# Kernel optimization log

Measured on AMD Instinct MI355X. Metric: run time of the kernel, lower is better.

## Reference

```python
import jax, jax.numpy as jnp
import numpy as np
import math

B, H, HK, Q, K, D = 2, 64, 8, 1024, 1024, 128
HIDDEN = H * D

def setup_inputs() -> dict:
    key = jax.random.key(0)
    k1, k2, k3, k4, k5 = jax.random.split(key, 5)
    xq = jax.random.normal(k1, (B, H, Q, D), dtype=jnp.float32)
    keys = jax.random.normal(k2, (B, HK, K, D), dtype=jnp.float32)
    values = jax.random.normal(k3, (B, HK, K, D), dtype=jnp.float32)
    attn_mask = jax.random.normal(k4, (B, 1, Q, K), dtype=jnp.float32)
    wo = jax.random.normal(k5, (HIDDEN, HIDDEN), dtype=jnp.float32) * 0.02
    return {"xq": xq, "keys": keys, "values": values, "attn_mask": attn_mask, "wo": wo}

def reference(xq, keys, values, attn_mask, wo):
    b, h, q, d = xq.shape
    hk = keys.shape[1]
    g = h // hk  # GQA group size
    scale = 1.0 / math.sqrt(d)
    # expand kv heads to match query heads (group_attn_matmul semantics)
    k = jnp.repeat(keys, g, axis=1)    # [b, h, K, d]
    v = jnp.repeat(values, g, axis=1)  # [b, h, K, d]
    attn = jnp.einsum('bhqd,bhkd->bhqk', xq, k) * scale + attn_mask
    attn = jax.nn.softmax(attn, axis=-1)
    out = jnp.einsum('bhqk,bhkd->bhqd', attn, v)
    # nlp_concat_heads: [b, h, q, d] -> [b, q, h*d]
    out = out.transpose(0, 2, 1, 3).reshape(b, q, h * d)
    return out @ wo
```

## Files before the change

### kernel.cpp

```cpp
#include <hip/hip_runtime.h>
#include <hip/hip_bf16.h>
#include <stdint.h>

#define NB   2
#define NH   64
#define NHK  8
#define SQ   1024
#define SK   1024
#define DH   128
#define HID  8192
#define MROWS 2048
#define NT   128

typedef unsigned short u16;
typedef __bf16 bf16_t;
typedef bf16_t bf16x8 __attribute__((ext_vector_type(8)));
typedef float  f32x4  __attribute__((ext_vector_type(4)));
typedef u16    u16x8  __attribute__((ext_vector_type(8)));
typedef u16    u16x4  __attribute__((ext_vector_type(4)));

#define DEV __device__ __forceinline__

DEV u16 f2bf(float f) {
  uint32_t u = __builtin_bit_cast(uint32_t, f);
  u += 0x7fffu + ((u >> 16) & 1u);
  return (u16)(u >> 16);
}

DEV float bf2f(u16 u) {
  return __builtin_bit_cast(float, (uint32_t)u << 16);
}

DEV bf16x8 pack8(const float* v) {
  u16x8 r;
#pragma unroll
  for (int i = 0; i < 8; ++i) r[i] = f2bf(v[i]);
  return __builtin_bit_cast(bf16x8, r);
}

DEV f32x4 mfma16(bf16x8 a, bf16x8 b, f32x4 c) {
  return __builtin_amdgcn_mfma_f32_16x16x32_bf16(a, b, c, 0, 0, 0);
}

DEV void gload_lds16(const void* g, void* l) {
  __builtin_amdgcn_global_load_lds(
      (const __attribute__((address_space(1))) void*)g,
      (__attribute__((address_space(3))) void*)l, 16, 0, 0);
}

#define BAR()  asm volatile("s_barrier" ::: "memory")
#define VMC(n) asm volatile("s_waitcnt vmcnt(" #n ")" ::: "memory")

__global__ __launch_bounds__(256) void k_prep(
    const float* __restrict__ wo, u16* __restrict__ wt,
    const float* __restrict__ keys, char* __restrict__ kf,
    const float* __restrict__ values, char* __restrict__ vf,
    const float* __restrict__ mask, u16* __restrict__ mb) {
  __shared__ float tile[64][65];
  const int bid = blockIdx.x;
  const int tid = threadIdx.x;

  if (bid < 16384) {
    const int k0 = (bid & 127) * 64;
    const int n0 = (bid >> 7) * 64;
    const int r  = tid >> 4, cg = tid & 15;
#pragma unroll
    for (int p = 0; p < 4; ++p) {
      int row = r + p * 16;
      float4 v = *(const float4*)(wo + (size_t)(k0 + row) * 8192 + n0 + cg * 4);
      *(float4*)&tile[row][cg * 4] = v;
    }
    __syncthreads();
#pragma unroll
    for (int p = 0; p < 4; ++p) {
      int row = r + p * 16;
      u16x4 ov;
      ov[0] = f2bf(tile[cg * 4 + 0][row]);
      ov[1] = f2bf(tile[cg * 4 + 1][row]);
      ov[2] = f2bf(tile[cg * 4 + 2][row]);
      ov[3] = f2bf(tile[cg * 4 + 3][row]);
      *(u16x4*)(wt + (size_t)(n0 + row) * 8192 + k0 + cg * 4) = ov;
    }
  } else if (bid < 17408) {
    int g = (bid - 16384) * 256 + tid;
    int l    = g & 63;
    int blk  = (g >> 6) & 15;
    int t    = (g >> 10) & 15;
    int head = g >> 14;
    int ni = blk >> 2, c = blk & 3;
    int row = t * 64 + ni * 16 + (l & 15);
    int col = c * 32 + (l >> 4) * 8;
    const float* src = keys + ((size_t)head * 1024 + row) * 128 + col;
    float tb[8];
    *(float4*)tb       = *(const float4*)src;
    *(float4*)(tb + 4) = *(const float4*)(src + 4);
    u16x8 r;
#pragma unroll
    for (int i = 0; i < 8; ++i) r[i] = f2bf(tb[i]);
    *(u16x8*)(kf + (size_t)g * 16) = r;
  } else if (bid < 18432) {
    int g = (bid - 17408) * 256 + tid;
    int l    = g & 63;
    int blk  = (g >> 6) & 15;
    int t    = (g >> 10) & 15;
    int head = g >> 14;
    int ks = blk >> 3, nd = blk & 7;
    int k0 = t * 64 + ks * 32 + (l >> 4) * 8;
    int d  = nd * 16 + (l & 15);
    const float* src = values + (size_t)head * 131072 + (size_t)k0 * 128 + d;
    u16x8 r;
#pragma unroll
    for (int j = 0; j < 8; ++j) r[j] = f2bf(src[j * 128]);
    *(u16x8*)(vf + (size_t)g * 16) = r;
  } else {
    int g = (bid - 18432) * 256 + tid;
    const float* src = mask + (size_t)g * 8;
    float tb[8];
    *(float4*)tb       = *(const float4*)src;
    *(float4*)(tb + 4) = *(const float4*)(src + 4);
    u16x8 r;
#pragma unroll
    for (int i = 0; i < 8; ++i) r[i] = f2bf(tb[i]);
    *(u16x8*)(mb + (size_t)g * 8) = r;
  }
}

__global__ __launch_bounds__(256) void k_attn(
    const float* __restrict__ xq, const char* __restrict__ kf_g,
    const char* __restrict__ vf_g, const u16* __restrict__ maskb,
    u16* __restrict__ abf) {
  __shared__ char smem[16384];
  const int bid = (blockIdx.x & 7) * 128 + (blockIdx.x >> 3);
  const int tid = threadIdx.x;

  const int b = bid >> 9;
  const int h = (bid >> 3) & 63;
  const int q0 = (bid & 7) * 128;
  const int hk = h >> 3;
  const int w = tid >> 6, l = tid & 63;
  const int lr = l & 15, lg = l >> 4;
  char* pbyte = smem + w * 4096;

  bf16x8 qf[2][4];
  {
    const float* qb = xq + (((size_t)(b * NH + h) * SQ) + q0 + w * 32) * DH;
#pragma unroll
    for (int mi = 0; mi < 2; ++mi)
#pragma unroll
      for (int c = 0; c < 4; ++c) {
        const float* qp = qb + (size_t)(mi * 16 + lr) * DH + c * 32 + lg * 8;
        float t[8];
        *(float4*)t       = *(const float4*)qp;
        *(float4*)(t + 4) = *(const float4*)(qp + 4);
        qf[mi][c] = pack8(t);
      }
  }

  f32x4 o[2][8];
#pragma unroll
  for (int mi = 0; mi < 2; ++mi)
#pragma unroll
    for (int nd = 0; nd < 8; ++nd) o[mi][nd] = (f32x4){0.f, 0.f, 0.f, 0.f};
  float mrun[2] = {-1e30f, -1e30f}, lrun[2] = {0.f, 0.f};

  const char* kb_base = kf_g + (size_t)(b * NHK + hk) * 262144 + l * 16;
  const char* vb_base = vf_g + (size_t)(b * NHK + hk) * 262144 + l * 16;
  const u16* mk0 = maskb + (size_t)b * SQ * SK +
                   (size_t)(q0 + w * 32 + lr) * SK + lg * 4;
  const float SCALE = 0.08838834764831845f;
  const float L2E   = 1.4426950408889634f;
  const int rswz = (lr & 7) << 4;

  for (int t = 0; t < 16; ++t) {
    const int kb = t * 64;
    const char* kt = kb_base + t * 16384;
    u16x4 mpre[2][4];
#pragma unroll
    for (int mi = 0; mi < 2; ++mi)
#pragma unroll
      for (int ni = 0; ni < 4; ++ni)
        mpre[mi][ni] = *(const u16x4*)(mk0 + (size_t)mi * 16 * SK + kb + ni * 16);

    f32x4 st[2][4];
#pragma unroll
    for (int mi = 0; mi < 2; ++mi)
#pragma unroll
      for (int ni = 0; ni < 4; ++ni) st[mi][ni] = (f32x4){0.f, 0.f, 0.f, 0.f};
    __builtin_amdgcn_s_setprio(1);
#pragma unroll
    for (int ni = 0; ni < 4; ++ni)
#pragma unroll
      for (int c = 0; c < 4; ++c) {
        bf16x8 kf = *(const bf16x8*)(kt + (ni * 4 + c) * 1024);
        st[0][ni] = mfma16(kf, qf[0][c], st[0][ni]);
        st[1][ni] = mfma16(kf, qf[1][c], st[1][ni]);
      }
    __builtin_amdgcn_s_setprio(0);

#pragma unroll
    for (int mi = 0; mi < 2; ++mi) {
      float x[4][4];
#pragma unroll
      for (int ni = 0; ni < 4; ++ni)
#pragma unroll
        for (int r = 0; r < 4; ++r)
          x[ni][r] = st[mi][ni][r] * SCALE + bf2f(mpre[mi][ni][r]);
      float v = fmaxf(fmaxf(x[0][0], x[0][1]), fmaxf(x[0][2], x[0][3]));
#pragma unroll
      for (int ni = 1; ni < 4; ++ni)
        v = fmaxf(v, fmaxf(fmaxf(x[ni][0], x[ni][1]),
                           fmaxf(x[ni][2], x[ni][3])));
      v = fmaxf(v, __shfl_xor(v, 16));
      v = fmaxf(v, __shfl_xor(v, 32));
      if (__any(v > mrun[mi] + 8.0f)) {
        float mnew = fmaxf(mrun[mi], v);
        float fac = exp2f((mrun[mi] - mnew) * L2E);
        lrun[mi] *= fac;
        mrun[mi] = mnew;
#pragma unroll
        for (int r = 0; r < 4; ++r) {
          float fr = __shfl(fac, lg * 4 + r);
#pragma unroll
          for (int nd = 0; nd < 8; ++nd) o[mi][nd][r] *= fr;
        }
      }
      float rs = 0.f;
      char* prow = pbyte + (mi * 16 + lr) * 128;
#pragma unroll
      for (int ni = 0; ni < 4; ++ni) {
        float p0 = exp2f((x[ni][0] - mrun[mi]) * L2E);
        float p1 = exp2f((x[ni][1] - mrun[mi]) * L2E);
        float p2 = exp2f((x[ni][2] - mrun[mi]) * L2E);
        float p3 = exp2f((x[ni][3] - mrun[mi]) * L2E);
        rs += (p0 + p1) + (p2 + p3);
        uint2 pk;
        pk.x = f2bf(p0) | ((uint32_t)f2bf(p1) << 16);
        pk.y = f2bf(p2) | ((uint32_t)f2bf(p3) << 16);
        *(uint2*)(prow + ((ni * 32 + lg * 8) ^ rswz)) = pk;
      }
      rs += __shfl_xor(rs, 16);
      rs += __shfl_xor(rs, 32);
      lrun[mi] += rs;
    }

    const char* vt = vb_base + t * 16384;
    __builtin_amdgcn_s_setprio(1);
#pragma unroll
    for (int ks = 0; ks < 2; ++ks) {
      bf16x8 pf0 = *(const bf16x8*)(pbyte + lr * 128 +
                                    ((ks * 64 + lg * 16) ^ rswz));
      bf16x8 pf1 = *(const bf16x8*)(pbyte + (16 + lr) * 128 +
                                    ((ks * 64 + lg * 16) ^ rswz));
#pragma unroll
      for (int nd = 0; nd < 8; ++nd) {
        bf16x8 vf = *(const bf16x8*)(vt + (ks * 8 + nd) * 1024);
        o[0][nd] = mfma16(pf0, vf, o[0][nd]);
        o[1][nd] = mfma16(pf1, vf, o[1][nd]);
      }
    }
    __builtin_amdgcn_s_setprio(0);
  }

#pragma unroll
  for (int mi = 0; mi < 2; ++mi) {
    float inv[4];
#pragma unroll
    for (int r = 0; r < 4; ++r) inv[r] = 1.0f / __shfl(lrun[mi], lg * 4 + r);
#pragma unroll
    for (int nd = 0; nd < 8; ++nd)
#pragma unroll
      for (int r = 0; r < 4; ++r) {
        int grow = q0 + w * 32 + mi * 16 + lg * 4 + r;
        size_t m = (size_t)b * SQ + grow;
        int col = h * DH + nd * 16 + lr;
        abf[m * HID + col] = f2bf(o[mi][nd][r] * inv[r]);
      }
  }
}

__global__ __launch_bounds__(512, 2) void k_gemm(const u16* __restrict__ A,
                                                 const u16* __restrict__ Bt,
                                                 float* __restrict__ C) {
  __shared__ char L[131072];
  const int bid = blockIdx.x;
  const int logical = (bid & 7) * 32 + (bid >> 3);
  const int m0 = (logical & 7) * 256;
  const int n0 = (logical >> 3) * 256;
  const int tid = threadIdx.x;
  const int w = tid >> 6, l = tid & 63;
  const int lr = l & 15, lg = l >> 4;
  const int wm = w >> 2, wn = w & 3;

  int srow[2], scol[2];
#pragma unroll
  for (int j = 0; j < 2; ++j) {
    int ch = j * 512 + tid;
    srow[j] = ch >> 3;
    scol[j] = (ch & 7) ^ (srow[j] & 7);
  }

  const char* Ab = (const char*)A;
  const char* Bb = (const char*)Bt;

#define STAGE(gb, row0, tt, dst) do {                                          \
    int kt_ = ((tt) < NT ? (tt) : 0) * 64;                                     \
    _Pragma("unroll")                                                          \
    for (int j_ = 0; j_ < 2; ++j_)                                             \
      gload_lds16((gb) + ((size_t)((row0) + srow[j_]) * 8192 + kt_ +           \
                          scol[j_] * 8) * 2,                                   \
                  (dst) + j_ * 8192 + (w << 10));                              \
  } while (0)

#define LDA(base, hs) do {                                                     \
    _Pragma("unroll")                                                          \
    for (int mi_ = 0; mi_ < 4; ++mi_) {                                        \
      int r_ = wm * 64 + mi_ * 16 + lr;                                        \
      _Pragma("unroll")                                                        \
      for (int ks_ = 0; ks_ < 2; ++ks_)                                        \
        bA[mi_][ks_] = *(const bf16x8*)(L + (base) + (hs) * 16384 + r_ * 128 + \
                        ((ks_ * 64 + lg * 16) ^ ((r_ & 7) << 4)));             \
    }                                                                          \
  } while (0)

#define LDB(dst, base, hs) do {                                                \
    _Pragma("unroll")                                                          \
    for (int ni_ = 0; ni_ < 2; ++ni_) {                                        \
      int r_ = wn * 32 + ni_ * 16 + lr;                                        \
      _Pragma("unroll")                                                        \
      for (int ks_ = 0; ks_ < 2; ++ks_)                                        \
        dst[ni_][ks_] = *(const bf16x8*)(L + (base) + 32768 + (hs) * 16384 +   \
                        r_ * 128 + ((ks_ * 64 + lg * 16) ^ ((r_ & 7) << 4)));  \
    }                                                                          \
  } while (0)

#define MM(mh, nh, BB) do {                                                    \
    __builtin_amdgcn_s_setprio(1);                                             \
    _Pragma("unroll")                                                          \
    for (int mi_ = 0; mi_ < 4; ++mi_)                                          \
      _Pragma("unroll")                                                        \
      for (int ni_ = 0; ni_ < 2; ++ni_)                                        \
        _Pragma("unroll")                                                      \
        for (int ks_ = 0; ks_ < 2; ++ks_)                                      \
          acc[mh][nh][mi_][ni_] =                                              \
              mfma16(bA[mi_][ks_], BB[ni_][ks_], acc[mh][nh][mi_][ni_]);       \
    __builtin_amdgcn_s_setprio(0);                                             \
  } while (0)

  f32x4 acc[2][2][4][2];
#pragma unroll
  for (int a1 = 0; a1 < 2; ++a1)
#pragma unroll
    for (int a2 = 0; a2 < 2; ++a2)
#pragma unroll
      for (int a3 = 0; a3 < 4; ++a3)
#pragma unroll
        for (int a4 = 0; a4 < 2; ++a4)
          acc[a1][a2][a3][a4] = (f32x4){0.f, 0.f, 0.f, 0.f};

  bf16x8 bA[4][2], bB0[2][2], bB1[2][2];

  STAGE(Ab, m0,       0, L + 0);
  STAGE(Bb, n0,       0, L + 32768);
  STAGE(Bb, n0 + 128, 0, L + 49152);
  STAGE(Ab, m0 + 128, 0, L + 16384);
  STAGE(Ab, m0,       1, L + 65536);
  STAGE(Bb, n0,       1, L + 65536 + 32768);
  STAGE(Bb, n0 + 128, 1, L + 65536 + 49152);
  VMC(6);
  BAR();

  for (int t = 0; t < NT; ++t) {
    const int c  = (t & 1) << 16;
    const int cn = c ^ 65536;
    STAGE(Ab, m0 + 128, t + 1, L + cn + 16384);
    LDA(c, 0);
    LDB(bB0, c, 0);
    BAR();
    MM(0, 0, bB0);
    BAR();
    STAGE(Ab, m0, t + 2, L + c + 0);
    LDB(bB1, c, 1);
    BAR();
    MM(0, 1, bB1);
    BAR();
    STAGE(Bb, n0, t + 2, L + c + 32768);
    LDA(c, 1);
    BAR();
    MM(1, 1, bB1);
    BAR();
    STAGE(Bb, n0 + 128, t + 2, L + c + 49152);
    BAR();
    MM(1, 0, bB0);
    VMC(6);
    BAR();
  }
  VMC(0);

#pragma unroll
  for (int mh = 0; mh < 2; ++mh)
#pragma unroll
    for (int nh = 0; nh < 2; ++nh)
#pragma unroll
      for (int mi = 0; mi < 4; ++mi)
#pragma unroll
        for (int ni = 0; ni < 2; ++ni)
#pragma unroll
          for (int rr = 0; rr < 4; ++rr)
            C[(size_t)(m0 + mh * 128 + wm * 64 + mi * 16 + lg * 4 + rr) * 8192 +
              n0 + nh * 128 + wn * 32 + ni * 16 + lr] = acc[mh][nh][mi][ni][rr];
#undef STAGE
#undef LDA
#undef LDB
#undef MM
}

extern "C" void kernel_launch(void* const* d_in, const int* in_sizes, int n_in,
                              void* d_out, int out_size, void* d_ws, size_t ws_size,
                              hipStream_t stream) {
  const float* xq     = (const float*)d_in[0];
  const float* keys   = (const float*)d_in[1];
  const float* values = (const float*)d_in[2];
  const float* mask   = (const float*)d_in[3];
  const float* wo     = (const float*)d_in[4];
  float* out = (float*)d_out;

  char* ws = (char*)d_ws;
  u16*  Abf = (u16*)ws;
  u16*  Wt  = (u16*)(ws + 33554432ull);
  char* Kf  = ws + 33554432ull + 134217728ull;
  char* Vf  = Kf + 4194304ull;
  u16*  Mb  = (u16*)((char*)d_out + 62914560ull);

  hipLaunchKernelGGL(k_prep, dim3(19456), dim3(256), 0, stream,
                     wo, Wt, keys, Kf, values, Vf, mask, Mb);
  hipLaunchKernelGGL(k_attn, dim3(1024), dim3(256), 0, stream,
                     xq, Kf, Vf, Mb, Abf);
  hipLaunchKernelGGL(k_gemm, dim3(256), dim3(512), 0, stream, Abf, Wt, out);
}
```

Before: 525.4 us.

## Double-buffer K/V tiles in LDS and fold log2e into mask and scale

Each workgroup now stages its K and V tiles into double-buffered shared memory with async global-to-LDS loads, prefetching tile t+1 while computing tile t. Before, every wave read K/V fragments straight from global memory. The log2(e) factor is folded into the mask conversion and the QK scale, which removes a multiply per exponent, and the rescale threshold is adjusted to match. The cost is 80KB of LDS per block, which may reduce occupancy, plus a barrier every iteration. The last iteration also prefetches a wrapped tile that is never used.

```diff
diff --git a/kernel.cpp b/kernel.cpp
--- a/kernel.cpp
+++ b/kernel.cpp
@@ -113,6 +113,7 @@
     for (int j = 0; j < 8; ++j) r[j] = f2bf(src[j * 128]);
     *(u16x8*)(vf + (size_t)g * 16) = r;
   } else {
+    const float L2E = 1.4426950408889634f;
     int g = (bid - 18432) * 256 + tid;
     const float* src = mask + (size_t)g * 8;
     float tb[8];
@@ -120,7 +121,7 @@
     *(float4*)(tb + 4) = *(const float4*)(src + 4);
     u16x8 r;
 #pragma unroll
-    for (int i = 0; i < 8; ++i) r[i] = f2bf(tb[i]);
+    for (int i = 0; i < 8; ++i) r[i] = f2bf(tb[i] * L2E);
     *(u16x8*)(mb + (size_t)g * 8) = r;
   }
 }
@@ -129,7 +130,9 @@
     const float* __restrict__ xq, const char* __restrict__ kf_g,
     const char* __restrict__ vf_g, const u16* __restrict__ maskb,
     u16* __restrict__ abf) {
-  __shared__ char smem[16384];
+  __shared__ char kbuf[2][16384];
+  __shared__ char vbuf[2][16384];
+  __shared__ char pls[16384];
   const int bid = (blockIdx.x & 7) * 128 + (blockIdx.x >> 3);
   const int tid = threadIdx.x;
 
@@ -139,7 +142,7 @@
   const int hk = h >> 3;
   const int w = tid >> 6, l = tid & 63;
   const int lr = l & 15, lg = l >> 4;
-  char* pbyte = smem + w * 4096;
+  char* pbyte = pls + w * 4096;
 
   bf16x8 qf[2][4];
   {
@@ -163,17 +166,28 @@
     for (int nd = 0; nd < 8; ++nd) o[mi][nd] = (f32x4){0.f, 0.f, 0.f, 0.f};
   float mrun[2] = {-1e30f, -1e30f}, lrun[2] = {0.f, 0.f};
 
-  const char* kb_base = kf_g + (size_t)(b * NHK + hk) * 262144 + l * 16;
-  const char* vb_base = vf_g + (size_t)(b * NHK + hk) * 262144 + l * 16;
+  const char* kf_h = kf_g + (size_t)(b * NHK + hk) * 262144 + l * 16;
+  const char* vf_h = vf_g + (size_t)(b * NHK + hk) * 262144 + l * 16;
   const u16* mk0 = maskb + (size_t)b * SQ * SK +
                    (size_t)(q0 + w * 32 + lr) * SK + lg * 4;
-  const float SCALE = 0.08838834764831845f;
-  const float L2E   = 1.4426950408889634f;
+  const float SCALE2 = 0.08838834764831845f * 1.4426950408889634f;
   const int rswz = (lr & 7) << 4;
 
+#define STG(src, tt, dst) do {                                                 \
+    const char* s_ = (src) + (((tt) & 15) * 16384);                            \
+    _Pragma("unroll")                                                          \
+    for (int j_ = 0; j_ < 4; ++j_)                                             \
+      gload_lds16(s_ + (w * 4 + j_) * 1024, (dst) + (w * 4 + j_) * 1024);      \
+  } while (0)
+
+  STG(kf_h, 0, kbuf[0]);
+  STG(vf_h, 0, vbuf[0]);
+  VMC(0);
+  BAR();
+
   for (int t = 0; t < 16; ++t) {
+    const int cur = t & 1;
     const int kb = t * 64;
-    const char* kt = kb_base + t * 16384;
     u16x4 mpre[2][4];
 #pragma unroll
     for (int mi = 0; mi < 2; ++mi)
@@ -181,6 +195,9 @@
       for (int ni = 0; ni < 4; ++ni)
         mpre[mi][ni] = *(const u16x4*)(mk0 + (size_t)mi * 16 * SK + kb + ni * 16);
 
+    STG(kf_h, t + 1, kbuf[cur ^ 1]);
+    STG(vf_h, t + 1, vbuf[cur ^ 1]);
+
     f32x4 st[2][4];
 #pragma unroll
     for (int mi = 0; mi < 2; ++mi)
@@ -191,9 +208,9 @@
     for (int ni = 0; ni < 4; ++ni)
 #pragma unroll
       for (int c = 0; c < 4; ++c) {
-        bf16x8 kf = *(const bf16x8*)(kt + (ni * 4 + c) * 1024);
-        st[0][ni] = mfma16(kf, qf[0][c], st[0][ni]);
-        st[1][ni] = mfma16(kf, qf[1][c], st[1][ni]);
+        bf16x8 kfr = *(const bf16x8*)(kbuf[cur] + (ni * 4 + c) * 1024 + l * 16);
+        st[0][ni] = mfma16(kfr, qf[0][c], st[0][ni]);
+        st[1][ni] = mfma16(kfr, qf[1][c], st[1][ni]);
       }
     __builtin_amdgcn_s_setprio(0);
 
@@ -204,7 +221,7 @@
       for (int ni = 0; ni < 4; ++ni)
 #pragma unroll
         for (int r = 0; r < 4; ++r)
-          x[ni][r] = st[mi][ni][r] * SCALE + bf2f(mpre[mi][ni][r]);
+          x[ni][r] = st[mi][ni][r] * SCALE2 + bf2f(mpre[mi][ni][r]);
       float v = fmaxf(fmaxf(x[0][0], x[0][1]), fmaxf(x[0][2], x[0][3]));
 #pragma unroll
       for (int ni = 1; ni < 4; ++ni)
@@ -212,9 +229,9 @@
                            fmaxf(x[ni][2], x[ni][3])));
       v = fmaxf(v, __shfl_xor(v, 16));
       v = fmaxf(v, __shfl_xor(v, 32));
-      if (__any(v > mrun[mi] + 8.0f)) {
+      if (__any(v > mrun[mi] + 11.5f)) {
         float mnew = fmaxf(mrun[mi], v);
-        float fac = exp2f((mrun[mi] - mnew) * L2E);
+        float fac = exp2f(mrun[mi] - mnew);
         lrun[mi] *= fac;
         mrun[mi] = mnew;
 #pragma unroll
@@ -228,10 +245,10 @@
       char* prow = pbyte + (mi * 16 + lr) * 128;
 #pragma unroll
       for (int ni = 0; ni < 4; ++ni) {
-        float p0 = exp2f((x[ni][0] - mrun[mi]) * L2E);
-        float p1 = exp2f((x[ni][1] - mrun[mi]) * L2E);
-        float p2 = exp2f((x[ni][2] - mrun[mi]) * L2E);
-        float p3 = exp2f((x[ni][3] - mrun[mi]) * L2E);
+        float p0 = exp2f(x[ni][0] - mrun[mi]);
+        float p1 = exp2f(x[ni][1] - mrun[mi]);
+        float p2 = exp2f(x[ni][2] - mrun[mi]);
+        float p3 = exp2f(x[ni][3] - mrun[mi]);
         rs += (p0 + p1) + (p2 + p3);
         uint2 pk;
         pk.x = f2bf(p0) | ((uint32_t)f2bf(p1) << 16);
@@ -243,7 +260,6 @@
       lrun[mi] += rs;
     }
 
-    const char* vt = vb_base + t * 16384;
     __builtin_amdgcn_s_setprio(1);
 #pragma unroll
     for (int ks = 0; ks < 2; ++ks) {
@@ -253,13 +269,17 @@
                                     ((ks * 64 + lg * 16) ^ rswz));
 #pragma unroll
       for (int nd = 0; nd < 8; ++nd) {
-        bf16x8 vf = *(const bf16x8*)(vt + (ks * 8 + nd) * 1024);
-        o[0][nd] = mfma16(pf0, vf, o[0][nd]);
-        o[1][nd] = mfma16(pf1, vf, o[1][nd]);
+        bf16x8 vfr = *(const bf16x8*)(vbuf[cur] + (ks * 8 + nd) * 1024 + l * 16);
+        o[0][nd] = mfma16(pf0, vfr, o[0][nd]);
+        o[1][nd] = mfma16(pf1, vfr, o[1][nd]);
       }
     }
     __builtin_amdgcn_s_setprio(0);
-  }
+
+    VMC(0);
+    BAR();
+  }
+#undef STG
 
 #pragma unroll
   for (int mi = 0; mi < 2; ++mi) {
```

Result: slower. 571.2 us (+8.7%).
